# Kernel tuning notes

Hardware: AMD Instinct MI355X
Metric: run time of the kernel (lower is better)

The kernel has to match this reference:

```python
import jax, jax.numpy as jnp
import numpy as np

EMBED_DIM = 384
HIDDEN_DIM = 512
CODEBOOK_SIZE = 256
NUM_QUANTIZERS = 4
COMMIT_WEIGHT = 0.25
BATCH = 65536


def setup_inputs() -> dict:
    key = jax.random.key(0)
    ks = jax.random.split(key, 10)
    s_in = 1.0 / np.sqrt(EMBED_DIM)
    s_h = 1.0 / np.sqrt(HIDDEN_DIM)
    return {
        "x": jax.random.normal(ks[0], (BATCH, EMBED_DIM), jnp.float32),
        "enc_w1": jax.random.uniform(ks[1], (EMBED_DIM, HIDDEN_DIM), jnp.float32, -s_in, s_in),
        "enc_b1": jnp.zeros((HIDDEN_DIM,), jnp.float32),
        "enc_w2": jax.random.uniform(ks[2], (HIDDEN_DIM, HIDDEN_DIM), jnp.float32, -s_h, s_h),
        "enc_b2": jnp.zeros((HIDDEN_DIM,), jnp.float32),
        "codebooks": jax.random.normal(ks[3], (NUM_QUANTIZERS, CODEBOOK_SIZE, HIDDEN_DIM), jnp.float32),
        "dec_w1": jax.random.uniform(ks[4], (HIDDEN_DIM, HIDDEN_DIM), jnp.float32, -s_h, s_h),
        "dec_b1": jnp.zeros((HIDDEN_DIM,), jnp.float32),
        "dec_w2": jax.random.uniform(ks[5], (HIDDEN_DIM, EMBED_DIM), jnp.float32, -s_h, s_h),
        "dec_b2": jnp.zeros((EMBED_DIM,), jnp.float32),
    }


def _residual_vq(z, codebooks):
    """Sequential residual VQ with straight-through estimator and commitment loss.
    z: [B, D]; codebooks: [Q, K, D]. Returns quantized [B, D], indices [B, Q], commit_loss scalar."""
    residual = z
    quantized_out = jnp.zeros_like(z)
    commit_loss = jnp.asarray(0.0, z.dtype)
    idx_list = []
    for q in range(NUM_QUANTIZERS):
        cb = codebooks[q]  # [K, D]
        # nearest code: argmin ||r - c||^2 == argmax (2 r.c - ||c||^2)
        scores = 2.0 * (residual @ cb.T) - jnp.sum(cb * cb, axis=-1)  # [B, K]
        idx = jnp.argmax(scores, axis=-1)  # [B]
        quant = cb[idx]  # [B, D] gather
        commit_loss = commit_loss + COMMIT_WEIGHT * jnp.mean(
            (residual - jax.lax.stop_gradient(quant)) ** 2)
        # straight-through: value = quant, gradient flows to residual
        quant_st = residual + jax.lax.stop_gradient(quant - residual)
        quantized_out = quantized_out + quant_st
        residual = residual - jax.lax.stop_gradient(quant)
        idx_list.append(idx)
    indices = jnp.stack(idx_list, axis=-1)  # [B, Q]
    return quantized_out, indices, commit_loss


def reference(x, enc_w1, enc_b1, enc_w2, enc_b2, codebooks,
              dec_w1, dec_b1, dec_w2, dec_b2):
    # encoder MLP
    z = jax.nn.relu(x @ enc_w1 + enc_b1) @ enc_w2 + enc_b2  # [B, H]
    quantized, indices, commit_loss = _residual_vq(z, codebooks)
    # decoder MLP
    recon = jax.nn.relu(quantized @ dec_w1 + dec_b1) @ dec_w2 + dec_b2  # [B, E]
    recon_loss = jnp.mean((recon - x) ** 2)
    return recon, indices, recon_loss, commit_loss
```

## Files before the change

kernel.cpp:

```cpp
#include <hip/hip_runtime.h>
#include <cfloat>
#include <cstddef>
#include <cstdint>


#define BATCH   65536
#define EDIM    384
#define HDIM    512
#define NCODE   256
#define NQ      4

#define OUT_IDX_OFF 25165824
#define OUT_RL_OFF  25427968
#define WS_P0       0
#define WS_P1       33554432
#define WS_CBW      67108864
#define WS_CNORM    67633152
#define WS_COMMITP  67634176
#define WS_RECONP   67636224
#define WS_W1S      67637760
#define WS_W2S      67834368
#define WS_W3S      68096512
#define WS_W4S      68358656
#define WS_CBA      68555264
#define WS_G6       69079552
#define WS_ZN       69472768
#define WS_SSTAR    69538304
#define WS_IDXI     69800448

typedef _Float16 half8 __attribute__((ext_vector_type(8)));
typedef float    f32x16 __attribute__((ext_vector_type(16)));

__device__ __forceinline__ void cvt_hl8(const float* vs, half8& h, half8& l)
{
#pragma unroll
    for (int j = 0; j < 8; ++j) {
        _Float16 hv = (_Float16)vs[j];
        h[j] = hv;
        l[j] = (_Float16)(vs[j] - (float)hv);
    }
}

__device__ __forceinline__ void gll16(const unsigned short* g, unsigned short* l)
{
    __builtin_amdgcn_global_load_lds(
        (const __attribute__((address_space(1))) unsigned int*)g,
        (__attribute__((address_space(3))) unsigned int*)l, 16, 0, 0);
}

template <int N> __device__ __forceinline__ void waitvm()
{
    __builtin_amdgcn_sched_barrier(0);
    if constexpr (N == 0)      asm volatile("s_waitcnt vmcnt(0)" ::: "memory");
    else if constexpr (N == 6) asm volatile("s_waitcnt vmcnt(6)" ::: "memory");
    __builtin_amdgcn_sched_barrier(0);
}
__device__ __forceinline__ void barrier_raw()
{
    __builtin_amdgcn_s_barrier();
    __builtin_amdgcn_sched_barrier(0);
}

__global__ __launch_bounds__(256)
void split_act(const float* __restrict__ src, unsigned short* __restrict__ dst,
               int K)
{
    int u = blockIdx.x * 256 + threadIdx.x;
    int upr = K >> 3;
    int row = u / upr;
    int rem = u % upr;
    int kt = rem >> 1, kh = rem & 1;
    const float* p = src + (size_t)row * K + kt * 16 + kh * 8;
    float vs[8];
#pragma unroll
    for (int j = 0; j < 8; ++j) vs[j] = p[j];
    half8 h, l;
    cvt_hl8(vs, h, l);
    unsigned short* o = dst + (size_t)row * (2 * K) + kt * 32 + kh * 8;
    *reinterpret_cast<half8*>(o)      = h;
    *reinterpret_cast<half8*>(o + 16) = l;
}

__global__ __launch_bounds__(256)
void split_w(const float* __restrict__ W, unsigned short* __restrict__ out,
             int N, int K)
{
    int u = blockIdx.x * 256 + threadIdx.x;
    int col  = u % N;
    int rem  = u / N;
    int khalf = rem & 1;
    int kt    = rem >> 1;
    int kbase = kt * 16 + khalf * 8;
    float vs[8];
#pragma unroll
    for (int j = 0; j < 8; ++j) vs[j] = W[(size_t)(kbase + j) * N + col];
    half8 h, l;
    cvt_hl8(vs, h, l);
    *reinterpret_cast<half8*>(out + ((size_t)(kt * 4 + khalf) * N + col) * 8)     = h;
    *reinterpret_cast<half8*>(out + ((size_t)(kt * 4 + 2 + khalf) * N + col) * 8) = l;
}

__global__ __launch_bounds__(256)
void split_cbw(const float* __restrict__ cb, unsigned short* __restrict__ out)
{
    int u = blockIdx.x * 256 + threadIdx.x;
    int col = u & 1023;
    int rem = u >> 10;
    int kh = rem & 1;
    int kt = rem >> 1;
    const float* p = cb + (size_t)col * HDIM + kt * 16 + kh * 8;
    float vs[8];
#pragma unroll
    for (int j = 0; j < 8; ++j) vs[j] = p[j];
    half8 h, l;
    cvt_hl8(vs, h, l);
    *reinterpret_cast<half8*>(out + ((size_t)(kt * 4 + kh) * 1024 + col) * 8)     = h;
    *reinterpret_cast<half8*>(out + ((size_t)(kt * 4 + 2 + kh) * 1024 + col) * 8) = l;
}

__global__ __launch_bounds__(64)
void cnorm_kernel(const float* __restrict__ cb, float* __restrict__ cnorm)
{
    const int code = blockIdx.x;
    const int lane = threadIdx.x;
    const float* r = cb + (size_t)code * HDIM;
    float s = 0.f;
    for (int k = lane; k < HDIM; k += 64) s = fmaf(r[k], r[k], s);
#pragma unroll
    for (int off = 32; off > 0; off >>= 1) s += __shfl_down(s, off);
    if (lane == 0) cnorm[code] = s;
}

__global__ __launch_bounds__(256)
void rownorm(const unsigned short* __restrict__ zs, float* __restrict__ zn)
{
    const int tid = threadIdx.x, wid = tid >> 6, lane = tid & 63;
    const int row = blockIdx.x * 4 + wid;
    const unsigned short* p = zs + (size_t)row * 1024
                                 + (lane >> 1) * 32 + (lane & 1) * 8;
    half8 h = *reinterpret_cast<const half8*>(p);
    half8 l = *reinterpret_cast<const half8*>(p + 16);
    float s = 0.f;
#pragma unroll
    for (int e = 0; e < 8; ++e) {
        float v = (float)h[e] + (float)l[e];
        s = fmaf(v, v, s);
    }
#pragma unroll
    for (int off = 32; off > 0; off >>= 1) s += __shfl_down(s, off);
    if (lane == 0) zn[row] = s;
}

template <int BN, int NKT, int OMODE, bool RELU>
__global__ __launch_bounds__(256, 2)
void gemm_pl(const unsigned short* __restrict__ Ain,
             const unsigned short* __restrict__ Wsp,
             const float* __restrict__ bias, void* __restrict__ Cout,
             const float* __restrict__ X, float* __restrict__ lossP,
             int N, int ldc)
{
    constexpr int WN  = BN / 128;
    constexpr int WM  = 4 / WN;
    constexpr int MR  = 128 / WM;
    constexpr int FM  = MR / 32;
    constexpr int K   = NKT * 16;
    constexpr int BOFF = 4096;
    constexpr int BUFU = 4096 + 4 * BN * 8;
    constexpr int NIB = BN / 64;

    __shared__ __align__(16) unsigned short lds[3][BUFU];

    const int tid  = threadIdx.x;
    const int wid  = tid >> 6;
    const int lane = tid & 63;
    const int l31  = lane & 31;
    const int lh   = lane >> 5;
    const int wm   = wid / WN;
    const int wn   = wid % WN;

    int bidx = blockIdx.y * gridDim.x + blockIdx.x;
    const int nwg = gridDim.x * gridDim.y;
    if ((nwg & 7) == 0) {
        const int cpx = nwg >> 3;
        bidx = (bidx & 7) * cpx + (bidx >> 3);
    }
    const int bx = bidx % gridDim.x;
    const int by = bidx / gridDim.x;
    const int row0 = by * 128;
    const int n0   = bx * BN;

    f32x16 acc[FM][4];
#pragma unroll
    for (int m = 0; m < FM; ++m)
#pragma unroll
        for (int n = 0; n < 4; ++n) acc[m][n] = (f32x16)(0.0f);

    auto stageB = [&](int buf, int kt) {
        const unsigned short* img = Wsp + (size_t)kt * 4 * N * 8;
        unsigned short* dstb = &lds[buf][BOFF];
#pragma unroll
        for (int t = 0; t < NIB; ++t) {
            int e = (wid * NIB + t) * 64 + lane;
            int u = (BN == 256) ? (e >> 8) : (e >> 7);
            int c = e & (BN - 1);
            gll16(img + ((size_t)u * N + n0 + c) * 8, dstb + (size_t)e * 8);
        }
    };
    auto stageA = [&](int buf, int kt) {
#pragma unroll
        for (int t = 0; t < 2; ++t) {
            int i = wid * 2 + t;
            int u = i >> 1, rh = i & 1;
            int row = rh * 64 + lane;
            gll16(Ain + (size_t)(row0 + row) * (2 * K) + kt * 32 + u * 8,
                  &lds[buf][(size_t)i * 512 + (size_t)lane * 8]);
        }
    };
    auto compute = [&](int buf) {
        const unsigned short* Ab = &lds[buf][0];
        const unsigned short* Bb = &lds[buf][BOFF];
        half8 Ah[FM], Al[FM];
#pragma unroll
        for (int fm = 0; fm < FM; ++fm) {
            int row = wm * MR + fm * 32 + l31;
            Ah[fm] = *reinterpret_cast<const half8*>(Ab + (size_t)lh * 1024 + (size_t)row * 8);
            Al[fm] = *reinterpret_cast<const half8*>(Ab + (size_t)(2 + lh) * 1024 + (size_t)row * 8);
        }
#pragma unroll
        for (int nt = 0; nt < 4; ++nt) {
            int col = wn * 128 + nt * 32 + l31;
            half8 Bh = *reinterpret_cast<const half8*>(Bb + (size_t)lh * BN * 8 + (size_t)col * 8);
            half8 Bl = *reinterpret_cast<const half8*>(Bb + (size_t)(2 + lh) * BN * 8 + (size_t)col * 8);
#pragma unroll
            for (int fm = 0; fm < FM; ++fm) {
                acc[fm][nt] = __builtin_amdgcn_mfma_f32_32x32x16_f16(Ah[fm], Bh, acc[fm][nt], 0, 0, 0);
                acc[fm][nt] = __builtin_amdgcn_mfma_f32_32x32x16_f16(Ah[fm], Bl, acc[fm][nt], 0, 0, 0);
                acc[fm][nt] = __builtin_amdgcn_mfma_f32_32x32x16_f16(Al[fm], Bh, acc[fm][nt], 0, 0, 0);
            }
        }
    };

    stageA(0, 0); stageB(0, 0);
    stageA(1, 1); stageB(1, 1);
    waitvm<6>();
    barrier_raw();
    for (int kt = 0; kt < NKT; ++kt) {
        const int cur = kt % 3;
        if (kt + 2 < NKT) { const int nb = (kt + 2) % 3; stageA(nb, kt + 2); stageB(nb, kt + 2); }
        compute(cur);
        if (kt < NKT - 2) waitvm<6>(); else waitvm<0>();
        barrier_raw();
    }

    if constexpr (OMODE == 0) {
        unsigned short* o = (unsigned short*)Cout;
        const size_t rs = (size_t)N * 2;
#pragma unroll
        for (int fm = 0; fm < FM; ++fm) {
#pragma unroll
            for (int nt = 0; nt < 4; ++nt) {
                const int col = n0 + wn * 128 + nt * 32 + l31;
                const float b = bias[col];
                const size_t cbo = (size_t)(col >> 4) * 32 + (size_t)((col >> 3) & 1) * 8 + (col & 7);
#pragma unroll
                for (int rg = 0; rg < 16; ++rg) {
                    const int row = row0 + wm * MR + fm * 32 + (rg & 3) + 8 * (rg >> 2) + 4 * lh;
                    float v = acc[fm][nt][rg] + b;
                    if (RELU) v = v > 0.f ? v : 0.f;
                    _Float16 hv = (_Float16)v;
                    _Float16 lv = (_Float16)(v - (float)hv);
                    union { _Float16 f; unsigned short u; } ch, cl;
                    ch.f = hv; cl.f = lv;
                    o[(size_t)row * rs + cbo]      = ch.u;
                    o[(size_t)row * rs + cbo + 16] = cl.u;
                }
            }
        }
    } else if constexpr (OMODE == 1) {
        float* C = (float*)Cout;
        float lacc = 0.f;
#pragma unroll
        for (int fm = 0; fm < FM; ++fm) {
#pragma unroll
            for (int nt = 0; nt < 4; ++nt) {
                const int col = n0 + wn * 128 + nt * 32 + l31;
                const float b = bias[col];
#pragma unroll
                for (int rg = 0; rg < 16; ++rg) {
                    const int row = row0 + wm * MR + fm * 32 + (rg & 3) + 8 * (rg >> 2) + 4 * lh;
                    float v = acc[fm][nt][rg] + b;
                    if (RELU) v = v > 0.f ? v : 0.f;
                    C[(size_t)row * N + col] = v;
                    float d = v - X[(size_t)row * N + col];
                    lacc = fmaf(d, d, lacc);
                }
            }
        }
        __shared__ float red[256];
        red[tid] = lacc;
        __syncthreads();
        for (int s = 128; s > 0; s >>= 1) {
            if (tid < s) red[tid] += red[tid + s];
            __syncthreads();
        }
        if (tid == 0) lossP[by * gridDim.x + bx] = red[0];
    } else {
        float* C = (float*)Cout;
#pragma unroll
        for (int fm = 0; fm < FM; ++fm) {
#pragma unroll
            for (int nt = 0; nt < 4; ++nt) {
                const int col = n0 + wn * 128 + nt * 32 + l31;
#pragma unroll
                for (int rg = 0; rg < 16; ++rg) {
                    const int row = row0 + wm * MR + fm * 32 + (rg & 3) + 8 * (rg >> 2) + 4 * lh;
                    C[(size_t)row * ldc + col] = acc[fm][nt][rg];
                }
            }
        }
    }
}

__global__ __launch_bounds__(256)
void vq_argmax(const float* __restrict__ S,
               const float* __restrict__ G6,
               const float* __restrict__ cnorm,
               float* __restrict__ idx_out,
               int* __restrict__ idxi,
               float* __restrict__ sstar,
               int rowbase)
{
    const int tid = threadIdx.x, wid = tid >> 6, lane = tid & 63;
    const int lrow = blockIdx.x * 4 + wid;
    const int grow = rowbase + lrow;
    const float* srow = S + (size_t)lrow * 1024;
    const int c0 = lane * 4;

    int iprev0 = 0, iprev1 = 0, iprev2 = 0;

#pragma unroll
    for (int q = 0; q < NQ; ++q) {
        float4 sv = *reinterpret_cast<const float4*>(srow + q * 256 + c0);
        float a[4] = {sv.x, sv.y, sv.z, sv.w};
        if (q >= 1) {
            const float* g = G6 + ((size_t)(q - 1) * 256 + iprev0) * 256 + c0;
            float4 gv = *reinterpret_cast<const float4*>(g);
            a[0] -= gv.x; a[1] -= gv.y; a[2] -= gv.z; a[3] -= gv.w;
        }
        if (q >= 2) {
            const float* g = G6 + ((size_t)(q + 1) * 256 + iprev1) * 256 + c0;
            float4 gv = *reinterpret_cast<const float4*>(g);
            a[0] -= gv.x; a[1] -= gv.y; a[2] -= gv.z; a[3] -= gv.w;
        }
        if (q >= 3) {
            const float* g = G6 + ((size_t)5 * 256 + iprev2) * 256 + c0;
            float4 gv = *reinterpret_cast<const float4*>(g);
            a[0] -= gv.x; a[1] -= gv.y; a[2] -= gv.z; a[3] -= gv.w;
        }
        float4 cnv = *reinterpret_cast<const float4*>(cnorm + q * 256 + c0);
        float cna[4] = {cnv.x, cnv.y, cnv.z, cnv.w};

        float bv = -FLT_MAX;
        int   bi = 0;
#pragma unroll
        for (int j = 0; j < 4; ++j) {
            float s = 2.f * a[j] - cna[j];
            const int code = c0 + j;
            if (s > bv || (s == bv && code < bi)) { bv = s; bi = code; }
        }
#pragma unroll
        for (int m = 1; m < 64; m <<= 1) {
            float ov = __shfl_xor(bv, m, 64);
            int   oi = __shfl_xor(bi, m, 64);
            if (ov > bv || (ov == bv && oi < bi)) { bv = ov; bi = oi; }
        }
        if (q == 0) iprev0 = bi;
        else if (q == 1) iprev1 = bi;
        else if (q == 2) iprev2 = bi;
        if (lane == 0) {
            idxi[q * 65536 + grow]  = bi;
            sstar[q * 65536 + grow] = bv;
            idx_out[(size_t)grow * NQ + q] = (float)bi;
        }
    }
}

__global__ __launch_bounds__(256)
void vq_quant(const int* __restrict__ idxi, const float* __restrict__ sstar,
              const float* __restrict__ zn, const float* __restrict__ cb,
              unsigned short* __restrict__ qout, float* __restrict__ commitP)
{
    __shared__ float red[256];
    const int tid = threadIdx.x, wid = tid >> 6, lane = tid & 63;
    float ca = 0.f;

#pragma unroll
    for (int t = 0; t < 8; ++t) {
        const int row = blockIdx.x * 32 + wid * 8 + t;
        const int i0 = idxi[row],          i1 = idxi[65536 + row];
        const int i2 = idxi[131072 + row], i3 = idxi[196608 + row];
        const int koff = lane * 8;
        const float* c0 = cb + ((size_t)(0 * NCODE + i0)) * HDIM + koff;
        const float* c1 = cb + ((size_t)(1 * NCODE + i1)) * HDIM + koff;
        const float* c2 = cb + ((size_t)(2 * NCODE + i2)) * HDIM + koff;
        const float* c3 = cb + ((size_t)(3 * NCODE + i3)) * HDIM + koff;
        float q[8];
#pragma unroll
        for (int half = 0; half < 2; ++half) {
            float4 v0 = *reinterpret_cast<const float4*>(c0 + half * 4);
            float4 v1 = *reinterpret_cast<const float4*>(c1 + half * 4);
            float4 v2 = *reinterpret_cast<const float4*>(c2 + half * 4);
            float4 v3 = *reinterpret_cast<const float4*>(c3 + half * 4);
            q[half * 4 + 0] = ((v0.x + v1.x) + v2.x) + v3.x;
            q[half * 4 + 1] = ((v0.y + v1.y) + v2.y) + v3.y;
            q[half * 4 + 2] = ((v0.z + v1.z) + v2.z) + v3.z;
            q[half * 4 + 3] = ((v0.w + v1.w) + v2.w) + v3.w;
        }
        half8 oh, ol;
        cvt_hl8(q, oh, ol);
        unsigned short* op = qout + (size_t)row * 1024
                                  + (lane >> 1) * 32 + (lane & 1) * 8;
        *reinterpret_cast<half8*>(op)      = oh;
        *reinterpret_cast<half8*>(op + 16) = ol;

        if (lane == 0) {
            float rn = zn[row];
            rn -= sstar[row];           float cm = rn;
            rn -= sstar[65536 + row];   cm += rn;
            rn -= sstar[131072 + row];  cm += rn;
            rn -= sstar[196608 + row];  cm += rn;
            ca += cm;
        }
    }

    red[tid] = ca;
    __syncthreads();
    for (int s = 128; s > 0; s >>= 1) {
        if (tid < s) red[tid] += red[tid + s];
        __syncthreads();
    }
    if (tid == 0) commitP[blockIdx.x] = red[0];
}

__global__ __launch_bounds__(256)
void loss_reduce(const float* __restrict__ cP, int nc,
                 const float* __restrict__ rP, int nr,
                 float* __restrict__ out2)
{
    __shared__ float red[256];
    const int tid = threadIdx.x;

    float s = 0.f;
    for (int i = tid; i < nc; i += 256) s += cP[i];
    red[tid] = s;
    __syncthreads();
    for (int st = 128; st > 0; st >>= 1) {
        if (tid < st) red[tid] += red[tid + st];
        __syncthreads();
    }
    float ctot = red[0];
    __syncthreads();

    s = 0.f;
    for (int i = tid; i < nr; i += 256) s += rP[i];
    red[tid] = s;
    __syncthreads();
    for (int st = 128; st > 0; st >>= 1) {
        if (tid < st) red[tid] += red[tid + st];
        __syncthreads();
    }
    if (tid == 0) {
        out2[0] = red[0] / ((float)BATCH * (float)EDIM);
        out2[1] = 0.25f * ctot / ((float)BATCH * (float)HDIM);
    }
}

extern "C" void kernel_launch(void* const* d_in, const int* in_sizes, int n_in,
                              void* d_out, int out_size, void* d_ws, size_t ws_size,
                              hipStream_t stream)
{
    const float* x   = (const float*)d_in[0];
    const float* ew1 = (const float*)d_in[1];
    const float* eb1 = (const float*)d_in[2];
    const float* ew2 = (const float*)d_in[3];
    const float* eb2 = (const float*)d_in[4];
    const float* cb  = (const float*)d_in[5];
    const float* dw1 = (const float*)d_in[6];
    const float* db1 = (const float*)d_in[7];
    const float* dw2 = (const float*)d_in[8];
    const float* db2 = (const float*)d_in[9];

    float* out = (float*)d_out;
    float* ws  = (float*)d_ws;
    unsigned short* P0  = (unsigned short*)(ws + WS_P0);
    unsigned short* P1  = (unsigned short*)(ws + WS_P1);
    unsigned short* XS  = P1;
    float* Sbuf = ws + WS_P0;
    unsigned short* cbw = (unsigned short*)(ws + WS_CBW);
    unsigned short* cba = (unsigned short*)(ws + WS_CBA);
    float* G6 = ws + WS_G6;
    float* zn = ws + WS_ZN;
    float* ss = ws + WS_SSTAR;
    int*   ii = (int*)(ws + WS_IDXI);
    float* cn = ws + WS_CNORM;
    float* cP = ws + WS_COMMITP;
    float* rP = ws + WS_RECONP;
    unsigned short* w1s = (unsigned short*)(ws + WS_W1S);
    unsigned short* w2s = (unsigned short*)(ws + WS_W2S);
    unsigned short* w3s = (unsigned short*)(ws + WS_W3S);
    unsigned short* w4s = (unsigned short*)(ws + WS_W4S);

    cnorm_kernel<<<NQ * NCODE, 64, 0, stream>>>(cb, cn);
    split_act<<<BATCH * 48 / 256, 256, 0, stream>>>(x, XS, EDIM);
    split_act<<<1024 * 64 / 256, 256, 0, stream>>>(cb, cba, HDIM);
    split_cbw<<<256, 256, 0, stream>>>(cb, cbw);
    split_w<<<(EDIM / 16) * 2 * HDIM / 256, 256, 0, stream>>>(ew1, w1s, HDIM, EDIM);
    split_w<<<(HDIM / 16) * 2 * HDIM / 256, 256, 0, stream>>>(ew2, w2s, HDIM, HDIM);
    split_w<<<(HDIM / 16) * 2 * HDIM / 256, 256, 0, stream>>>(dw1, w3s, HDIM, HDIM);
    split_w<<<(HDIM / 16) * 2 * EDIM / 256, 256, 0, stream>>>(dw2, w4s, EDIM, HDIM);

    {
        const int pairs[6][2] = {{0,1},{0,2},{0,3},{1,2},{1,3},{2,3}};
        for (int pi = 0; pi < 6; ++pi) {
            const int p = pairs[pi][0], q = pairs[pi][1];
            gemm_pl<256, 32, 2, false><<<dim3(1, 2), 256, 0, stream>>>(
                cba + (size_t)p * 256 * 1024, cbw + (size_t)q * 256 * 8,
                nullptr, G6 + (size_t)pi * 65536, nullptr, nullptr, 1024, 256);
        }
    }

    gemm_pl<256, 24, 0, true><<<dim3(HDIM / 256, BATCH / 128), 256, 0, stream>>>(
        XS, w1s, eb1, P0, nullptr, nullptr, HDIM, HDIM);
    gemm_pl<256, 32, 0, false><<<dim3(HDIM / 256, BATCH / 128), 256, 0, stream>>>(
        P0, w2s, eb2, P1, nullptr, nullptr, HDIM, HDIM);

    rownorm<<<BATCH / 4, 256, 0, stream>>>(P1, zn);

    float* idxo = out + OUT_IDX_OFF;
    for (int half = 0; half < 2; ++half) {
        const int rowbase = half * 32768;
        gemm_pl<256, 32, 2, false><<<dim3(4, 256), 256, 0, stream>>>(
            P1 + (size_t)rowbase * 1024, cbw, nullptr, Sbuf,
            nullptr, nullptr, 1024, 1024);
        vq_argmax<<<8192, 256, 0, stream>>>(Sbuf, G6, cn, idxo, ii, ss, rowbase);
    }

    vq_quant<<<BATCH / 32, 256, 0, stream>>>(ii, ss, zn, cb, P0, cP);

    gemm_pl<256, 32, 0, true><<<dim3(HDIM / 256, BATCH / 128), 256, 0, stream>>>(
        P0, w3s, db1, P1, nullptr, nullptr, HDIM, HDIM);
    gemm_pl<128, 32, 1, false><<<dim3(EDIM / 128, BATCH / 128), 256, 0, stream>>>(
        P1, w4s, db2, out, x, rP, EDIM, EDIM);

    loss_reduce<<<1, 256, 0, stream>>>(cP, BATCH / 32, rP,
                                       (BATCH / 128) * (EDIM / 128),
                                       out + OUT_RL_OFF);
}
```

Measured before the change: 968.7 us.

## Enlarge GEMM tiles to 256 rows with 512-thread blocks and fuse prep launches

The GEMM kernel moves from 128-row, 4-wave tiles to 256-row, 8-wave tiles (512 threads) with a 64-column per-wave split. Each block loads more A rows per B tile, which improves reuse of the staged B tile and halves the number of row blocks. The six weight and codebook split kernels are merged into one launch, and the six codebook-pair Gram GEMMs become a single launch using a new output mode. In exchange, LDS use per block doubles and there is more register pressure at two blocks per CU, which could reduce occupancy or cause spilling.

```diff
diff --git a/kernel.cpp b/kernel.cpp
--- a/kernel.cpp
+++ b/kernel.cpp
@@ -52,6 +52,8 @@
 {
     __builtin_amdgcn_sched_barrier(0);
     if constexpr (N == 0)      asm volatile("s_waitcnt vmcnt(0)" ::: "memory");
+    else if constexpr (N == 3) asm volatile("s_waitcnt vmcnt(3)" ::: "memory");
+    else if constexpr (N == 4) asm volatile("s_waitcnt vmcnt(4)" ::: "memory");
     else if constexpr (N == 6) asm volatile("s_waitcnt vmcnt(6)" ::: "memory");
     __builtin_amdgcn_sched_barrier(0);
 }
@@ -81,29 +83,28 @@
     *reinterpret_cast<half8*>(o + 16) = l;
 }
 
-__global__ __launch_bounds__(256)
-void split_w(const float* __restrict__ W, unsigned short* __restrict__ out,
-             int N, int K)
-{
-    int u = blockIdx.x * 256 + threadIdx.x;
+__device__ __forceinline__ void body_split_w(const float* __restrict__ W,
+                                             unsigned short* __restrict__ out,
+                                             int N, int u)
+{
     int col  = u % N;
     int rem  = u / N;
-    int khalf = rem & 1;
-    int kt    = rem >> 1;
-    int kbase = kt * 16 + khalf * 8;
+    int kh   = rem & 1;
+    int kt   = rem >> 1;
+    int kbase = kt * 16 + kh * 8;
     float vs[8];
 #pragma unroll
     for (int j = 0; j < 8; ++j) vs[j] = W[(size_t)(kbase + j) * N + col];
     half8 h, l;
     cvt_hl8(vs, h, l);
-    *reinterpret_cast<half8*>(out + ((size_t)(kt * 4 + khalf) * N + col) * 8)     = h;
-    *reinterpret_cast<half8*>(out + ((size_t)(kt * 4 + 2 + khalf) * N + col) * 8) = l;
-}
-
-__global__ __launch_bounds__(256)
-void split_cbw(const float* __restrict__ cb, unsigned short* __restrict__ out)
-{
-    int u = blockIdx.x * 256 + threadIdx.x;
+    *reinterpret_cast<half8*>(out + ((size_t)(kt * 4 + kh) * N + col) * 8)     = h;
+    *reinterpret_cast<half8*>(out + ((size_t)(kt * 4 + 2 + kh) * N + col) * 8) = l;
+}
+
+__device__ __forceinline__ void body_split_cbw(const float* __restrict__ cb,
+                                               unsigned short* __restrict__ out,
+                                               int u)
+{
     int col = u & 1023;
     int rem = u >> 10;
     int kh = rem & 1;
@@ -116,6 +117,41 @@
     cvt_hl8(vs, h, l);
     *reinterpret_cast<half8*>(out + ((size_t)(kt * 4 + kh) * 1024 + col) * 8)     = h;
     *reinterpret_cast<half8*>(out + ((size_t)(kt * 4 + 2 + kh) * 1024 + col) * 8) = l;
+}
+
+__device__ __forceinline__ void body_split_cba(const float* __restrict__ cb,
+                                               unsigned short* __restrict__ out,
+                                               int u)
+{
+    int row = u >> 6;
+    int rem = u & 63;
+    int kt = rem >> 1, kh = rem & 1;
+    const float* p = cb + (size_t)row * HDIM + kt * 16 + kh * 8;
+    float vs[8];
+#pragma unroll
+    for (int j = 0; j < 8; ++j) vs[j] = p[j];
+    half8 h, l;
+    cvt_hl8(vs, h, l);
+    unsigned short* o = out + (size_t)row * 1024 + kt * 32 + kh * 8;
+    *reinterpret_cast<half8*>(o)      = h;
+    *reinterpret_cast<half8*>(o + 16) = l;
+}
+
+__global__ __launch_bounds__(256)
+void split_wall(const float* __restrict__ ew1, const float* __restrict__ ew2,
+                const float* __restrict__ dw1, const float* __restrict__ dw2,
+                const float* __restrict__ cb,
+                unsigned short* __restrict__ w1s, unsigned short* __restrict__ w2s,
+                unsigned short* __restrict__ w3s, unsigned short* __restrict__ w4s,
+                unsigned short* __restrict__ cbw, unsigned short* __restrict__ cba)
+{
+    const int b = blockIdx.x, tid = threadIdx.x;
+    if (b < 96)        body_split_w(ew1, w1s, HDIM, b * 256 + tid);
+    else if (b < 224)  body_split_w(ew2, w2s, HDIM, (b - 96) * 256 + tid);
+    else if (b < 352)  body_split_w(dw1, w3s, HDIM, (b - 224) * 256 + tid);
+    else if (b < 448)  body_split_w(dw2, w4s, EDIM, (b - 352) * 256 + tid);
+    else if (b < 704)  body_split_cbw(cb, cbw, (b - 448) * 256 + tid);
+    else               body_split_cba(cb, cba, (b - 704) * 256 + tid);
 }
 
 __global__ __launch_bounds__(64)
@@ -152,21 +188,21 @@
 }
 
 template <int BN, int NKT, int OMODE, bool RELU>
-__global__ __launch_bounds__(256, 2)
+__global__ __launch_bounds__(512, 2)
 void gemm_pl(const unsigned short* __restrict__ Ain,
              const unsigned short* __restrict__ Wsp,
              const float* __restrict__ bias, void* __restrict__ Cout,
              const float* __restrict__ X, float* __restrict__ lossP,
              int N, int ldc)
 {
-    constexpr int WN  = BN / 128;
-    constexpr int WM  = 4 / WN;
-    constexpr int MR  = 128 / WM;
+    constexpr int WN  = BN / 64;
+    constexpr int WM  = 8 / WN;
+    constexpr int MR  = 256 / WM;
     constexpr int FM  = MR / 32;
     constexpr int K   = NKT * 16;
-    constexpr int BOFF = 4096;
-    constexpr int BUFU = 4096 + 4 * BN * 8;
-    constexpr int NIB = BN / 64;
+    constexpr int BOFF = 8192;
+    constexpr int BUFU = 8192 + 32 * BN;
+    constexpr int GPI  = 2 + ((BN == 256) ? 2 : 1);
 
     __shared__ __align__(16) unsigned short lds[3][BUFU];
 
@@ -178,42 +214,61 @@
     const int wm   = wid / WN;
     const int wn   = wid % WN;
 
-    int bidx = blockIdx.y * gridDim.x + blockIdx.x;
-    const int nwg = gridDim.x * gridDim.y;
-    if ((nwg & 7) == 0) {
-        const int cpx = nwg >> 3;
-        bidx = (bidx & 7) * cpx + (bidx >> 3);
-    }
-    const int bx = bidx % gridDim.x;
-    const int by = bidx / gridDim.x;
-    const int row0 = by * 128;
-    const int n0   = bx * BN;
-
-    f32x16 acc[FM][4];
+    int row0, n0, bx = 0, by = 0, pair = 0;
+    const unsigned short* Abase = Ain;
+    if constexpr (OMODE == 3) {
+        const int ptab[6] = {0, 0, 0, 1, 1, 2};
+        const int qtab[6] = {1, 2, 3, 2, 3, 3};
+        pair = blockIdx.x;
+        Abase = Ain + (size_t)ptab[pair] * 256 * 1024;
+        row0 = 0;
+        n0   = qtab[pair] * 256;
+    } else {
+        int bidx = blockIdx.y * gridDim.x + blockIdx.x;
+        const int nwg = gridDim.x * gridDim.y;
+        if ((nwg & 7) == 0) {
+            const int cpx = nwg >> 3;
+            bidx = (bidx & 7) * cpx + (bidx >> 3);
+        }
+        bx = bidx % gridDim.x;
+        by = bidx / gridDim.x;
+        row0 = by * 256;
+        n0   = bx * BN;
+    }
+
+    f32x16 acc[FM][2];
 #pragma unroll
     for (int m = 0; m < FM; ++m)
 #pragma unroll
-        for (int n = 0; n < 4; ++n) acc[m][n] = (f32x16)(0.0f);
-
+        for (int n = 0; n < 2; ++n) acc[m][n] = (f32x16)(0.0f);
+
+    auto stageA = [&](int buf, int kt) {
+#pragma unroll
+        for (int t = 0; t < 2; ++t) {
+            const int i = t * 8 + wid;
+            const int u = i >> 2;
+            const int row = (i & 3) * 64 + lane;
+            gll16(Abase + (size_t)(row0 + row) * (2 * K) + kt * 32 + u * 8,
+                  &lds[buf][(size_t)i * 512 + (size_t)lane * 8]);
+        }
+    };
     auto stageB = [&](int buf, int kt) {
         const unsigned short* img = Wsp + (size_t)kt * 4 * N * 8;
         unsigned short* dstb = &lds[buf][BOFF];
-#pragma unroll
-        for (int t = 0; t < NIB; ++t) {
-            int e = (wid * NIB + t) * 64 + lane;
-            int u = (BN == 256) ? (e >> 8) : (e >> 7);
-            int c = e & (BN - 1);
-            gll16(img + ((size_t)u * N + n0 + c) * 8, dstb + (size_t)e * 8);
-        }
-    };
-    auto stageA = [&](int buf, int kt) {
-#pragma unroll
-        for (int t = 0; t < 2; ++t) {
-            int i = wid * 2 + t;
-            int u = i >> 1, rh = i & 1;
-            int row = rh * 64 + lane;
-            gll16(Ain + (size_t)(row0 + row) * (2 * K) + kt * 32 + u * 8,
-                  &lds[buf][(size_t)i * 512 + (size_t)lane * 8]);
+        if constexpr (BN == 256) {
+#pragma unroll
+            for (int t = 0; t < 2; ++t) {
+                const int i = t * 8 + wid;
+                const int u = i >> 2;
+                const int col = (i & 3) * 64 + lane;
+                gll16(img + ((size_t)u * N + n0 + col) * 8,
+                      dstb + (size_t)i * 512 + (size_t)lane * 8);
+            }
+        } else {
+            const int u = wid >> 1;
+            const int col = (wid & 1) * 64 + lane;
+            gll16(img + ((size_t)u * N + n0 + col) * 8,
+                  dstb + (size_t)wid * 512 + (size_t)lane * 8);
         }
     };
     auto compute = [&](int buf) {
@@ -222,15 +277,15 @@
         half8 Ah[FM], Al[FM];
 #pragma unroll
         for (int fm = 0; fm < FM; ++fm) {
-            int row = wm * MR + fm * 32 + l31;
-            Ah[fm] = *reinterpret_cast<const half8*>(Ab + (size_t)lh * 1024 + (size_t)row * 8);
-            Al[fm] = *reinterpret_cast<const half8*>(Ab + (size_t)(2 + lh) * 1024 + (size_t)row * 8);
-        }
-#pragma unroll
-        for (int nt = 0; nt < 4; ++nt) {
-            int col = wn * 128 + nt * 32 + l31;
-            half8 Bh = *reinterpret_cast<const half8*>(Bb + (size_t)lh * BN * 8 + (size_t)col * 8);
-            half8 Bl = *reinterpret_cast<const half8*>(Bb + (size_t)(2 + lh) * BN * 8 + (size_t)col * 8);
+            const int row = wm * MR + fm * 32 + l31;
+            Ah[fm] = *reinterpret_cast<const half8*>(Ab + ((size_t)lh * 256 + row) * 8);
+            Al[fm] = *reinterpret_cast<const half8*>(Ab + ((size_t)(2 + lh) * 256 + row) * 8);
+        }
+#pragma unroll
+        for (int nt = 0; nt < 2; ++nt) {
+            const int col = wn * 64 + nt * 32 + l31;
+            half8 Bh = *reinterpret_cast<const half8*>(Bb + ((size_t)lh * BN + col) * 8);
+            half8 Bl = *reinterpret_cast<const half8*>(Bb + ((size_t)(2 + lh) * BN + col) * 8);
 #pragma unroll
             for (int fm = 0; fm < FM; ++fm) {
                 acc[fm][nt] = __builtin_amdgcn_mfma_f32_32x32x16_f16(Ah[fm], Bh, acc[fm][nt], 0, 0, 0);
@@ -242,13 +297,13 @@
 
     stageA(0, 0); stageB(0, 0);
     stageA(1, 1); stageB(1, 1);
-    waitvm<6>();
+    waitvm<GPI>();
     barrier_raw();
     for (int kt = 0; kt < NKT; ++kt) {
         const int cur = kt % 3;
         if (kt + 2 < NKT) { const int nb = (kt + 2) % 3; stageA(nb, kt + 2); stageB(nb, kt + 2); }
         compute(cur);
-        if (kt < NKT - 2) waitvm<6>(); else waitvm<0>();
+        if (kt < NKT - 2) waitvm<GPI>(); else waitvm<0>();
         barrier_raw();
     }
 
@@ -258,8 +313,8 @@
 #pragma unroll
         for (int fm = 0; fm < FM; ++fm) {
 #pragma unroll
-            for (int nt = 0; nt < 4; ++nt) {
-                const int col = n0 + wn * 128 + nt * 32 + l31;
+            for (int nt = 0; nt < 2; ++nt) {
+                const int col = n0 + wn * 64 + nt * 32 + l31;
                 const float b = bias[col];
                 const size_t cbo = (size_t)(col >> 4) * 32 + (size_t)((col >> 3) & 1) * 8 + (col & 7);
 #pragma unroll
@@ -282,8 +337,8 @@
 #pragma unroll
         for (int fm = 0; fm < FM; ++fm) {
 #pragma unroll
-            for (int nt = 0; nt < 4; ++nt) {
-                const int col = n0 + wn * 128 + nt * 32 + l31;
+            for (int nt = 0; nt < 2; ++nt) {
+                const int col = n0 + wn * 64 + nt * 32 + l31;
                 const float b = bias[col];
 #pragma unroll
                 for (int rg = 0; rg < 16; ++rg) {
@@ -296,25 +351,39 @@
                 }
             }
         }
-        __shared__ float red[256];
+        __shared__ float red[512];
         red[tid] = lacc;
         __syncthreads();
-        for (int s = 128; s > 0; s >>= 1) {
+        for (int s = 256; s > 0; s >>= 1) {
             if (tid < s) red[tid] += red[tid + s];
             __syncthreads();
         }
         if (tid == 0) lossP[by * gridDim.x + bx] = red[0];
-    } else {
+    } else if constexpr (OMODE == 2) {
         float* C = (float*)Cout;
 #pragma unroll
         for (int fm = 0; fm < FM; ++fm) {
 #pragma unroll
-            for (int nt = 0; nt < 4; ++nt) {
-                const int col = n0 + wn * 128 + nt * 32 + l31;
+            for (int nt = 0; nt < 2; ++nt) {
+                const int col = n0 + wn * 64 + nt * 32 + l31;
 #pragma unroll
                 for (int rg = 0; rg < 16; ++rg) {
                     const int row = row0 + wm * MR + fm * 32 + (rg & 3) + 8 * (rg >> 2) + 4 * lh;
                     C[(size_t)row * ldc + col] = acc[fm][nt][rg];
+                }
+            }
+        }
+    } else {
+        float* C = (float*)Cout + (size_t)pair * 65536;
+#pragma unroll
+        for (int fm = 0; fm < FM; ++fm) {
+#pragma unroll
+            for (int nt = 0; nt < 2; ++nt) {
+                const int colL = wn * 64 + nt * 32 + l31;
+#pragma unroll
+                for (int rg = 0; rg < 16; ++rg) {
+                    const int row = wm * MR + fm * 32 + (rg & 3) + 8 * (rg >> 2) + 4 * lh;
+                    C[(size_t)row * 256 + colL] = acc[fm][nt][rg];
                 }
             }
         }
@@ -406,15 +475,15 @@
         const float* c3 = cb + ((size_t)(3 * NCODE + i3)) * HDIM + koff;
         float q[8];
 #pragma unroll
-        for (int half = 0; half < 2; ++half) {
-            float4 v0 = *reinterpret_cast<const float4*>(c0 + half * 4);
-            float4 v1 = *reinterpret_cast<const float4*>(c1 + half * 4);
-            float4 v2 = *reinterpret_cast<const float4*>(c2 + half * 4);
-            float4 v3 = *reinterpret_cast<const float4*>(c3 + half * 4);
-            q[half * 4 + 0] = ((v0.x + v1.x) + v2.x) + v3.x;
-            q[half * 4 + 1] = ((v0.y + v1.y) + v2.y) + v3.y;
-            q[half * 4 + 2] = ((v0.z + v1.z) + v2.z) + v3.z;
-            q[half * 4 + 3] = ((v0.w + v1.w) + v2.w) + v3.w;
+        for (int hh = 0; hh < 2; ++hh) {
+            float4 v0 = *reinterpret_cast<const float4*>(c0 + hh * 4);
+            float4 v1 = *reinterpret_cast<const float4*>(c1 + hh * 4);
+            float4 v2 = *reinterpret_cast<const float4*>(c2 + hh * 4);
+            float4 v3 = *reinterpret_cast<const float4*>(c3 + hh * 4);
+            q[hh * 4 + 0] = ((v0.x + v1.x) + v2.x) + v3.x;
+            q[hh * 4 + 1] = ((v0.y + v1.y) + v2.y) + v3.y;
+            q[hh * 4 + 2] = ((v0.z + v1.z) + v2.z) + v3.z;
+            q[hh * 4 + 3] = ((v0.w + v1.w) + v2.w) + v3.w;
         }
         half8 oh, ol;
         cvt_hl8(q, oh, ol);
@@ -512,26 +581,15 @@
 
     cnorm_kernel<<<NQ * NCODE, 64, 0, stream>>>(cb, cn);
     split_act<<<BATCH * 48 / 256, 256, 0, stream>>>(x, XS, EDIM);
-    split_act<<<1024 * 64 / 256, 256, 0, stream>>>(cb, cba, HDIM);
-    split_cbw<<<256, 256, 0, stream>>>(cb, cbw);
-    split_w<<<(EDIM / 16) * 2 * HDIM / 256, 256, 0, stream>>>(ew1, w1s, HDIM, EDIM);
-    split_w<<<(HDIM / 16) * 2 * HDIM / 256, 256, 0, stream>>>(ew2, w2s, HDIM, HDIM);
-    split_w<<<(HDIM / 16) * 2 * HDIM / 256, 256, 0, stream>>>(dw1, w3s, HDIM, HDIM);
-    split_w<<<(HDIM / 16) * 2 * EDIM / 256, 256, 0, stream>>>(dw2, w4s, EDIM, HDIM);
-
-    {
-        const int pairs[6][2] = {{0,1},{0,2},{0,3},{1,2},{1,3},{2,3}};
-        for (int pi = 0; pi < 6; ++pi) {
-            const int p = pairs[pi][0], q = pairs[pi][1];
-            gemm_pl<256, 32, 2, false><<<dim3(1, 2), 256, 0, stream>>>(
-                cba + (size_t)p * 256 * 1024, cbw + (size_t)q * 256 * 8,
-                nullptr, G6 + (size_t)pi * 65536, nullptr, nullptr, 1024, 256);
-        }
-    }
-
-    gemm_pl<256, 24, 0, true><<<dim3(HDIM / 256, BATCH / 128), 256, 0, stream>>>(
+    split_wall<<<960, 256, 0, stream>>>(ew1, ew2, dw1, dw2, cb,
+                                        w1s, w2s, w3s, w4s, cbw, cba);
+
+    gemm_pl<256, 32, 3, false><<<dim3(6, 1), 512, 0, stream>>>(
+        cba, cbw, nullptr, G6, nullptr, nullptr, 1024, 256);
+
+    gemm_pl<256, 24, 0, true><<<dim3(HDIM / 256, BATCH / 256), 512, 0, stream>>>(
         XS, w1s, eb1, P0, nullptr, nullptr, HDIM, HDIM);
-    gemm_pl<256, 32, 0, false><<<dim3(HDIM / 256, BATCH / 128), 256, 0, stream>>>(
+    gemm_pl<256, 32, 0, false><<<dim3(HDIM / 256, BATCH / 256), 512, 0, stream>>>(
         P0, w2s, eb2, P1, nullptr, nullptr, HDIM, HDIM);
 
     rownorm<<<BATCH / 4, 256, 0, stream>>>(P1, zn);
@@ -539,7 +597,7 @@
     float* idxo = out + OUT_IDX_OFF;
     for (int half = 0; half < 2; ++half) {
         const int rowbase = half * 32768;
-        gemm_pl<256, 32, 2, false><<<dim3(4, 256), 256, 0, stream>>>(
+        gemm_pl<256, 32, 2, false><<<dim3(4, 128), 512, 0, stream>>>(
             P1 + (size_t)rowbase * 1024, cbw, nullptr, Sbuf,
             nullptr, nullptr, 1024, 1024);
         vq_argmax<<<8192, 256, 0, stream>>>(Sbuf, G6, cn, idxo, ii, ss, rowbase);
@@ -547,12 +605,12 @@
 
     vq_quant<<<BATCH / 32, 256, 0, stream>>>(ii, ss, zn, cb, P0, cP);
 
-    gemm_pl<256, 32, 0, true><<<dim3(HDIM / 256, BATCH / 128), 256, 0, stream>>>(
+    gemm_pl<256, 32, 0, true><<<dim3(HDIM / 256, BATCH / 256), 512, 0, stream>>>(
         P0, w3s, db1, P1, nullptr, nullptr, HDIM, HDIM);
-    gemm_pl<128, 32, 1, false><<<dim3(EDIM / 128, BATCH / 128), 256, 0, stream>>>(
+    gemm_pl<128, 32, 1, false><<<dim3(EDIM / 128, BATCH / 256), 512, 0, stream>>>(
         P1, w4s, db2, out, x, rP, EDIM, EDIM);
 
     loss_reduce<<<1, 256, 0, stream>>>(cP, BATCH / 32, rP,
-                                       (BATCH / 128) * (EDIM / 128),
+                                       (EDIM / 128) * (BATCH / 256),
                                        out + OUT_RL_OFF);
 }
```

After: 891.8 us. -7.9%, faster.
